# Optimization experiments

Hardware: AMD Instinct MI355X
Metric: run time of the kernel (lower is better)

Reference implementation:

```python
import jax, jax.numpy as jnp
import numpy as np

H, KV, D, HID, FF = 32, 8, 128, 4096, 14336
EPS = 1e-5
ROPE_THETA = 1e9


def setup_inputs() -> dict:
    key = jax.random.key(0)
    ks = jax.random.split(key, 10)
    B, S = 1, 2048
    s = 0.02
    return {
        "hidden_states": jax.random.normal(ks[0], (B, S, HID), dtype=jnp.float32),
        "wq": jax.random.normal(ks[1], (HID, H * D), dtype=jnp.float32) * s,
        "wk": jax.random.normal(ks[2], (HID, KV * D), dtype=jnp.float32) * s,
        "wv": jax.random.normal(ks[3], (HID, KV * D), dtype=jnp.float32) * s,
        "wo": jax.random.normal(ks[4], (H * D, HID), dtype=jnp.float32) * s,
        "w_gate": jax.random.normal(ks[5], (HID, FF), dtype=jnp.float32) * s,
        "w_up": jax.random.normal(ks[6], (HID, FF), dtype=jnp.float32) * s,
        "w_down": jax.random.normal(ks[7], (FF, HID), dtype=jnp.float32) * s,
        "ln1_w": jnp.ones((HID,), dtype=jnp.float32),
        "ln2_w": jnp.ones((HID,), dtype=jnp.float32),
        "position_ids": jnp.arange(B * S, dtype=jnp.int32).reshape(B, S),
    }


def _rmsnorm(x, w):
    var = jnp.mean(jnp.square(x), axis=-1, keepdims=True)
    return x * jax.lax.rsqrt(var + EPS) * w


def _rope_cos_sin(position_ids):
    inv_freq = 1.0 / (ROPE_THETA ** (jnp.arange(0, D, 2, dtype=jnp.float32) / D))  # [D/2]
    ang = position_ids.astype(jnp.float32)[..., None] * inv_freq  # [B,S,D/2]
    ang = jnp.concatenate([ang, ang], axis=-1)  # [B,S,D]
    return jnp.cos(ang), jnp.sin(ang)


def _rotate_half(x):
    x1, x2 = x[..., : D // 2], x[..., D // 2:]
    return jnp.concatenate([-x2, x1], axis=-1)


def _apply_rope(x, cos, sin):
    # x: [B,S,h,D]; cos/sin: [B,S,D]
    c, s = cos[:, :, None, :], sin[:, :, None, :]
    return x * c + _rotate_half(x) * s


def reference(hidden_states, wq, wk, wv, wo, w_gate, w_up, w_down, ln1_w, ln2_w, position_ids):
    B, S, _ = hidden_states.shape
    G = H // KV  # query groups per kv head

    # --- attention block ---
    residual = hidden_states
    x = _rmsnorm(hidden_states, ln1_w)
    q = (x @ wq).reshape(B, S, H, D)
    k = (x @ wk).reshape(B, S, KV, D)
    v = (x @ wv).reshape(B, S, KV, D)

    cos, sin = _rope_cos_sin(position_ids)
    q = _apply_rope(q, cos, sin)
    k = _apply_rope(k, cos, sin)

    # GQA: group query heads over kv heads, [B,S,KV,G,D]
    qg = q.reshape(B, S, KV, G, D)
    scores = jnp.einsum("bqhgd,bkhd->bhgqk", qg, k) / jnp.sqrt(jnp.float32(D))
    causal = position_ids[:, :, None] >= position_ids[:, None, :]  # [B,S,S]
    scores = jnp.where(causal[:, None, None, :, :], scores, jnp.float32(-1e9))
    probs = jax.nn.softmax(scores, axis=-1)
    attn = jnp.einsum("bhgqk,bkhd->bqhgd", probs, v).reshape(B, S, H * D)
    hidden_states = residual + attn @ wo

    # --- MLP block (SwiGLU) ---
    residual = hidden_states
    x = _rmsnorm(hidden_states, ln2_w)
    mlp = (jax.nn.silu(x @ w_gate) * (x @ w_up)) @ w_down
    return residual + mlp
```

## Files before the change

### kernel.cpp

```cpp
#include <hip/hip_runtime.h>

typedef short bf16x8 __attribute__((ext_vector_type(8)));
typedef float f32x4 __attribute__((ext_vector_type(4)));

#define DEV __device__ __forceinline__

constexpr int SEQ = 2048;
constexpr int HID = 4096;
constexpr int NH  = 32;
constexpr int NKV = 8;
constexpr int DH  = 128;
constexpr int FF  = 14336;
constexpr int QKVN = NH * DH + 2 * NKV * DH;

DEV unsigned short f2bf(float f) {
  union { float f; unsigned u; } x; x.f = f;
  unsigned r = x.u + 0x7fffu + ((x.u >> 16) & 1u);
  return (unsigned short)(r >> 16);
}
DEV float bf2f(unsigned short u) {
  union { unsigned u; float f; } x; x.u = ((unsigned)u) << 16; return x.f;
}
DEV void gload16(const void* g, void* l) {
  __builtin_amdgcn_global_load_lds(
      (const __attribute__((address_space(1))) unsigned*)g,
      (__attribute__((address_space(3))) unsigned*)l, 16, 0, 0);
}

DEV void wtrans_tail(char* smbase, int tid, int tile0, int stride,
                     const float* __restrict__ TW,
                     unsigned short* __restrict__ TWT, int TK, int TN) {
  const int team = tid >> 8, lt = tid & 255;
  unsigned short(*tt)[72] = (unsigned short(*)[72])(smbase + team * 9216);
  const int tilesK = TK >> 6;
  const int tot = tilesK * (TN >> 6);
  const int tk = lt >> 4;
  const int tn4 = (lt & 15) * 4;
  for (int tile = tile0 * 2 + team; tile < tot; tile += stride * 2) {
    const int k0 = (tile % tilesK) << 6;
    const int n0t = (tile / tilesK) << 6;
#pragma unroll
    for (int p = 0; p < 4; ++p) {
      int k = tk + p * 16;
      float4 v = *(const float4*)(TW + (size_t)(k0 + k) * TN + n0t + tn4);
      tt[tn4 + 0][k] = f2bf(v.x);
      tt[tn4 + 1][k] = f2bf(v.y);
      tt[tn4 + 2][k] = f2bf(v.z);
      tt[tn4 + 3][k] = f2bf(v.w);
    }
    __syncthreads();
#pragma unroll
    for (int p = 0; p < 4; ++p) {
      int n = tk + p * 16;
      ushort4 o = *(const ushort4*)&tt[n][tn4];
      *(ushort4*)(TWT + (size_t)(n0t + n) * TK + k0 + tn4) = o;
    }
    __syncthreads();
  }
}

__global__ __launch_bounds__(256) void rmsnorm_kernel(
    const float* __restrict__ x, const float* __restrict__ w,
    unsigned short* __restrict__ out) {
  const int row = blockIdx.x;
  const int tid = threadIdx.x;
  const float* xr = x + (size_t)row * HID;
  float4 v[4];
  float ss = 0.f;
#pragma unroll
  for (int i = 0; i < 4; ++i) {
    v[i] = *(const float4*)(xr + i * 1024 + tid * 4);
    ss += v[i].x * v[i].x + v[i].y * v[i].y + v[i].z * v[i].z + v[i].w * v[i].w;
  }
#pragma unroll
  for (int m = 1; m < 64; m <<= 1) ss += __shfl_xor(ss, m);
  __shared__ float red[4];
  if ((tid & 63) == 0) red[tid >> 6] = ss;
  __syncthreads();
  float tot = red[0] + red[1] + red[2] + red[3];
  float rms = rsqrtf(tot / (float)HID + 1e-5f);
  unsigned short* orow = out + (size_t)row * HID;
#pragma unroll
  for (int i = 0; i < 4; ++i) {
    int base = i * 1024 + tid * 4;
    ushort4 o;
    o.x = f2bf(v[i].x * rms * w[base + 0]);
    o.y = f2bf(v[i].y * rms * w[base + 1]);
    o.z = f2bf(v[i].z * rms * w[base + 2]);
    o.w = f2bf(v[i].w * rms * w[base + 3]);
    *(ushort4*)(orow + base) = o;
  }
}

__global__ __launch_bounds__(256) void wtrans_kernel(
    const float* __restrict__ W, unsigned short* __restrict__ WT, int K,
    int N) {
  __shared__ unsigned short t[64][72];
  const int k0 = blockIdx.x * 64, n0 = blockIdx.y * 64;
  const int tid = threadIdx.x;
  const int tk = tid >> 4;
  const int tn4 = (tid & 15) * 4;
#pragma unroll
  for (int p = 0; p < 4; ++p) {
    int k = tk + p * 16;
    float4 v = *(const float4*)(W + (size_t)(k0 + k) * N + n0 + tn4);
    t[tn4 + 0][k] = f2bf(v.x);
    t[tn4 + 1][k] = f2bf(v.y);
    t[tn4 + 2][k] = f2bf(v.z);
    t[tn4 + 3][k] = f2bf(v.w);
  }
  __syncthreads();
#pragma unroll
  for (int p = 0; p < 4; ++p) {
    int n = tk + p * 16;
    ushort4 o = *(const ushort4*)&t[n][tn4];
    *(ushort4*)(WT + (size_t)(n0 + n) * K + k0 + tn4) = o;
  }
}

__global__ __launch_bounds__(256) void rope_kernel(unsigned short* __restrict__ x,
                                                   int nheads, int ld) {
  const int gid = blockIdx.x * 256 + threadIdx.x;
  const int i = gid & 63;
  const int t = gid >> 6;
  const int s = t / nheads;
  const int hh = t - s * nheads;
  float ang = (float)s * exp2f((float)i * (-29.897352853986263f / 64.f));
  float sn, cs;
  sincosf(ang, &sn, &cs);
  size_t base = (size_t)s * ld + hh * DH + i;
  float x1 = bf2f(x[base]);
  float x2 = bf2f(x[base + 64]);
  x[base]      = f2bf(x1 * cs - x2 * sn);
  x[base + 64] = f2bf(x2 * cs + x1 * sn);
}

__global__ __launch_bounds__(256) void combine_kernel(
    const float* __restrict__ p0, const float* __restrict__ p1,
    const float* __restrict__ res, float* __restrict__ out) {
  const size_t i = ((size_t)blockIdx.x * 256 + threadIdx.x) * 4;
  float4 a = *(const float4*)(p0 + i);
  float4 b = *(const float4*)(p1 + i);
  float4 c = *(const float4*)(res + i);
  float4 o;
  o.x = a.x + b.x + c.x;
  o.y = a.y + b.y + c.y;
  o.z = a.z + b.z + c.z;
  o.w = a.w + b.w + c.w;
  *(float4*)(out + i) = o;
}

__global__ __launch_bounds__(256) void combine_rms_kernel(
    const float* __restrict__ p0, const float* __restrict__ p1,
    const float* __restrict__ res, const float* __restrict__ w,
    float* __restrict__ h2, unsigned short* __restrict__ xn2) {
  const int row = blockIdx.x;
  const int tid = threadIdx.x;
  const size_t base = (size_t)row * HID;
  float4 h[4];
  float ss = 0.f;
#pragma unroll
  for (int i = 0; i < 4; ++i) {
    size_t idx = base + i * 1024 + tid * 4;
    float4 a = *(const float4*)(p0 + idx);
    float4 b = *(const float4*)(p1 + idx);
    float4 c = *(const float4*)(res + idx);
    h[i].x = a.x + b.x + c.x;
    h[i].y = a.y + b.y + c.y;
    h[i].z = a.z + b.z + c.z;
    h[i].w = a.w + b.w + c.w;
    *(float4*)(h2 + idx) = h[i];
    ss += h[i].x * h[i].x + h[i].y * h[i].y + h[i].z * h[i].z + h[i].w * h[i].w;
  }
#pragma unroll
  for (int m = 1; m < 64; m <<= 1) ss += __shfl_xor(ss, m);
  __shared__ float red[4];
  if ((tid & 63) == 0) red[tid >> 6] = ss;
  __syncthreads();
  float tot = red[0] + red[1] + red[2] + red[3];
  float rms = rsqrtf(tot / (float)HID + 1e-5f);
#pragma unroll
  for (int i = 0; i < 4; ++i) {
    int off = i * 1024 + tid * 4;
    ushort4 o;
    o.x = f2bf(h[i].x * rms * w[off + 0]);
    o.y = f2bf(h[i].y * rms * w[off + 1]);
    o.z = f2bf(h[i].z * rms * w[off + 2]);
    o.w = f2bf(h[i].w * rms * w[off + 3]);
    *(ushort4*)(xn2 + base + off) = o;
  }
}

template <int EPI>
__global__ __launch_bounds__(512, 2) void gemm8p_kernel(
    const unsigned short* __restrict__ A, const unsigned short* __restrict__ BT,
    void* __restrict__ Cv0, void* __restrict__ Cv1, int gridM, int N, int Kld,
    int nsplit, const float* __restrict__ TW, unsigned short* __restrict__ TWT,
    int TK, int TN, int n_t) {
  constexpr int MF = 4;
  constexpr int ABYTES = 256 * 128;
  constexpr int BUFBYTES = ABYTES + 32768;
  __shared__ __align__(128) char sm[2 * BUFBYTES];

  const int tid = threadIdx.x;
  const int nwg = gridDim.x - n_t;

  if ((int)blockIdx.x >= nwg) {
    wtrans_tail(sm, tid, (int)blockIdx.x - nwg, n_t, TW, TWT, TK, TN);
    return;
  }

  const int lane = tid & 63;
  const int wv   = tid >> 6;
  const int b = blockIdx.x;
  const int logical = (b & 7) * (nwg >> 3) + (b >> 3);
  const int ntiles = nwg / nsplit;
  const int s = logical / ntiles;
  const int r = logical - s * ntiles;
  const int m0 = (r % gridM) * 256;
  const int n0 = (r / gridM) * 256;
  const int Klen = Kld / nsplit;
  const int koff = s * Klen;
  const int wm = (wv >> 2) * 128;
  const int wn = (wv & 3) * 64;
  const int nt = Klen >> 6;

  const int srow = tid >> 3;
  const int scolb = (tid & 7) * 16;
  const int sldsbase = wv * 1024;

  auto stage = [&](int h, int t) {
    const int buf = t & 1;
    const int kt = koff + t * 64;
    char* ldsOp;
    const unsigned short* g;
    int grow0, rowBase;
    if (h < 2) {
      ldsOp = sm + buf * BUFBYTES + ABYTES; g = BT; grow0 = n0; rowBase = h * 128;
    } else {
      ldsOp = sm + buf * BUFBYTES;          g = A;  grow0 = m0; rowBase = (h - 2) * 128;
    }
#pragma unroll
    for (int rr = 0; rr < 2; ++rr) {
      int row = rowBase + rr * 64 + srow;
      const char* gp = (const char*)g + ((size_t)(grow0 + row) * Kld + kt) * 2 +
                       (scolb ^ ((row & 7) << 4));
      gload16(gp, ldsOp + rowBase * 128 + rr * 8192 + sldsbase);
    }
  };

  const int kb0 = (lane >> 4) * 16;
  const int lrow = lane & 15;
  auto ldA = [&](const char* sA, int mh, int mf, int ks) {
    int row = wm + mh * 64 + mf * 16 + lrow;
    return *(const bf16x8*)(sA + ((row * 128 + kb0 + ks * 64) ^ ((row & 7) << 4)));
  };
  auto ldB = [&](const char* sB, int j, int ks) {
    int col = wn + j * 16 + lrow;
    return *(const bf16x8*)(sB + ((col * 128 + kb0 + ks * 64) ^ ((col & 7) << 4)));
  };

  f32x4 acc[2 * MF][4] = {};

  stage(2, 0); stage(3, 0); stage(0, 0); stage(1, 0);
  if (nt > 1) {
    stage(0, 1); stage(1, 1);
    asm volatile("s_waitcnt vmcnt(4)" ::: "memory");
  } else {
    asm volatile("s_waitcnt vmcnt(0)" ::: "memory");
  }
  __builtin_amdgcn_s_barrier();

  for (int t = 0; t < nt; ++t) {
    const char* sA = sm + (t & 1) * BUFBYTES;
    const char* sB = sA + ABYTES;
    bf16x8 a[MF], bb[4][2];

#pragma unroll
    for (int j = 0; j < 4; ++j) bb[j][0] = ldB(sB, j, 0);
#pragma unroll
    for (int mf = 0; mf < MF; ++mf) a[mf] = ldA(sA, 0, mf, 0);
    if (t + 1 < nt) stage(2, t + 1);
    __builtin_amdgcn_sched_barrier(0);
    __builtin_amdgcn_s_barrier();
    __builtin_amdgcn_s_setprio(1);
#pragma unroll
    for (int mf = 0; mf < MF; ++mf)
#pragma unroll
      for (int j = 0; j < 4; ++j)
        acc[mf][j] = __builtin_amdgcn_mfma_f32_16x16x32_bf16(
            a[mf], bb[j][0], acc[mf][j], 0, 0, 0);
    __builtin_amdgcn_s_setprio(0);
    __builtin_amdgcn_sched_barrier(0);
    __builtin_amdgcn_s_barrier();

#pragma unroll
    for (int j = 0; j < 4; ++j) bb[j][1] = ldB(sB, j, 1);
#pragma unroll
    for (int mf = 0; mf < MF; ++mf) a[mf] = ldA(sA, 0, mf, 1);
    if (t + 1 < nt) stage(3, t + 1);
    __builtin_amdgcn_sched_barrier(0);
    __builtin_amdgcn_s_barrier();
    __builtin_amdgcn_s_setprio(1);
#pragma unroll
    for (int mf = 0; mf < MF; ++mf)
#pragma unroll
      for (int j = 0; j < 4; ++j)
        acc[mf][j] = __builtin_amdgcn_mfma_f32_16x16x32_bf16(
            a[mf], bb[j][1], acc[mf][j], 0, 0, 0);
    __builtin_amdgcn_s_setprio(0);
    __builtin_amdgcn_sched_barrier(0);
    __builtin_amdgcn_s_barrier();

#pragma unroll
    for (int mf = 0; mf < MF; ++mf) a[mf] = ldA(sA, 1, mf, 0);
    if (t + 2 < nt) stage(0, t + 2);
    __builtin_amdgcn_sched_barrier(0);
    __builtin_amdgcn_s_barrier();
    __builtin_amdgcn_s_setprio(1);
#pragma unroll
    for (int mf = 0; mf < MF; ++mf)
#pragma unroll
      for (int j = 0; j < 4; ++j)
        acc[MF + mf][j] = __builtin_amdgcn_mfma_f32_16x16x32_bf16(
            a[mf], bb[j][0], acc[MF + mf][j], 0, 0, 0);
    __builtin_amdgcn_s_setprio(0);
    __builtin_amdgcn_sched_barrier(0);
    __builtin_amdgcn_s_barrier();

#pragma unroll
    for (int mf = 0; mf < MF; ++mf) a[mf] = ldA(sA, 1, mf, 1);
    if (t + 2 < nt) {
      stage(1, t + 2);
      asm volatile("s_waitcnt vmcnt(4)" ::: "memory");
    } else {
      asm volatile("s_waitcnt vmcnt(0)" ::: "memory");
    }
    __builtin_amdgcn_sched_barrier(0);
    __builtin_amdgcn_s_barrier();
    __builtin_amdgcn_s_setprio(1);
#pragma unroll
    for (int mf = 0; mf < MF; ++mf)
#pragma unroll
      for (int j = 0; j < 4; ++j)
        acc[MF + mf][j] = __builtin_amdgcn_mfma_f32_16x16x32_bf16(
            a[mf], bb[j][1], acc[MF + mf][j], 0, 0, 0);
    __builtin_amdgcn_s_setprio(0);
    __builtin_amdgcn_sched_barrier(0);
    __builtin_amdgcn_s_barrier();
  }

  const int rb = (lane >> 4) * 4;
  float* P = (float*)(s ? Cv1 : Cv0);
#pragma unroll
  for (int i = 0; i < 2 * MF; ++i) {
    const int mh = i / MF, mf = i % MF;
#pragma unroll
    for (int j = 0; j < 4; ++j) {
#pragma unroll
      for (int rr = 0; rr < 4; ++rr) {
        size_t row = (size_t)(m0 + wm + mh * 64 + mf * 16 + rb + rr);
        size_t col = (size_t)(n0 + wn + j * 16 + lrow);
        float vv = acc[i][j][rr];
        if (EPI == 0) {
          ((unsigned short*)Cv0)[row * N + col] = f2bf(vv);
        } else if (EPI == 2) {
          P[row * N + col] = vv;
        } else {
          float g = bf2f(((const unsigned short*)Cv1)[row * N + col]);
          float sl = g / (1.f + __expf(-g));
          ((unsigned short*)Cv0)[row * N + col] = f2bf(sl * vv);
        }
      }
    }
  }
}

__global__ __launch_bounds__(512, 1) void attn_kernel(
    const unsigned short* __restrict__ QKV, unsigned short* __restrict__ Ob,
    const float* __restrict__ TW, unsigned short* __restrict__ TWT, int TK,
    int TN, int n_t) {
  __shared__ __align__(128) char sm[114688];
  const int tid  = threadIdx.x;
  const int nattn = gridDim.x - n_t;
  if ((int)blockIdx.x >= nattn) {
    wtrans_tail(sm, tid, (int)blockIdx.x - nattn, n_t, TW, TWT, TK, TN);
    return;
  }
  char* sQ  = sm;
  char* sK0 = sm + 32768;
  char* sK1 = sm + 49152;
  char* sV0 = sm + 65536;
  char* sV1 = sm + 81920;
  char* sP  = sm + 98304;
  const int lane = tid & 63;
  const int wv   = tid >> 6;
  const int logical = blockIdx.x;
  const int xr = 15 - (logical >> 5);
  const int h = logical & 31;
  const int qb0 = xr * 128;
  const int hkv = h >> 2;
  const int rbase = (lane >> 4) * 4;
  const int cbase = lane & 15;
  const unsigned short* Qp = QKV + h * DH;
  const unsigned short* Kp = QKV + NH * DH + hkv * DH;
  const unsigned short* Vp = QKV + NH * DH + NKV * DH + hkv * DH;

#pragma unroll
  for (int i = 0; i < 4; ++i) {
    int offs = i * 8192 + tid * 16;
    int row = offs >> 8, col = offs & 255;
    const char* gp = (const char*)Qp + ((size_t)(qb0 + row) * QKVN) * 2 +
                     (col ^ ((row & 15) << 4));
    gload16(gp, sQ + i * 8192 + wv * 1024);
  }

  auto stageK = [&](int t) {
    char* dst = (t & 1) ? sK1 : sK0;
    const int kt0 = t * 64;
#pragma unroll
    for (int i = 0; i < 2; ++i) {
      int offs = i * 8192 + tid * 16;
      int row = offs >> 8, col = offs & 255;
      const char* gp = (const char*)Kp + ((size_t)(kt0 + row) * QKVN) * 2 +
                       (col ^ ((row & 15) << 4));
      gload16(gp, dst + i * 8192 + wv * 1024);
    }
  };

  const int d4  = (tid & 31) * 4;
  const int kv4 = (tid >> 5) * 4;
  const int rot = (tid >> 1) & 3;
  auto loadV = [&](int t, ushort4* vr) {
    const unsigned short* g0 = Vp + (size_t)(t * 64 + kv4) * QKVN + d4;
#pragma unroll
    for (int k = 0; k < 4; ++k) vr[k] = *(const ushort4*)(g0 + (size_t)k * QKVN);
  };
  auto writeV = [&](int t, const ushort4* vr) {
    char* dst = (t & 1) ? sV1 : sV0;
    const unsigned short* a0 = (const unsigned short*)&vr[0];
    const unsigned short* a1 = (const unsigned short*)&vr[1];
    const unsigned short* a2 = (const unsigned short*)&vr[2];
    const unsigned short* a3 = (const unsigned short*)&vr[3];
#pragma unroll
    for (int j = 0; j < 4; ++j) {
      int jj = (j + rot) & 3;
      int dd = d4 + jj;
      uint2 pk;
      pk.x = (unsigned)a0[jj] | ((unsigned)a1[jj] << 16);
      pk.y = (unsigned)a2[jj] | ((unsigned)a3[jj] << 16);
      *(uint2*)(dst + ((dd * 128 + kv4 * 2) ^ ((dd & 7) << 4))) = pk;
    }
  };

  ushort4 vr[4];
  stageK(0);
  loadV(0, vr);
  asm volatile("s_waitcnt vmcnt(0)" ::: "memory");
  writeV(0, vr);
  __syncthreads();

  const int qrow = wv * 16 + (lane & 15);
  bf16x8 aq[4];
#pragma unroll
  for (int kk = 0; kk < 4; ++kk) {
    int kb = (lane >> 4) * 16 + kk * 64;
    aq[kk] = *(const bf16x8*)(sQ + ((qrow * 256 + kb) ^ ((qrow & 15) << 4)));
  }

  f32x4 oacc[8] = {};
  float m_r[4] = {-1e30f, -1e30f, -1e30f, -1e30f};
  float l_r[4] = {0.f, 0.f, 0.f, 0.f};
  const int ntiles = 2 * (xr + 1);

  for (int t = 0; t < ntiles; ++t) {
    const int kt0 = t * 64;
    const char* cK = (t & 1) ? sK1 : sK0;
    const char* cV = (t & 1) ? sV1 : sV0;
    if (t + 1 < ntiles) {
      stageK(t + 1);
      loadV(t + 1, vr);
    }

    f32x4 sacc[4] = {};
#pragma unroll
    for (int kk = 0; kk < 4; ++kk) {
      int kb = (lane >> 4) * 16 + kk * 64;
#pragma unroll
      for (int ni = 0; ni < 4; ++ni) {
        int krow = ni * 16 + (lane & 15);
        bf16x8 bk =
            *(const bf16x8*)(cK + ((krow * 256 + kb) ^ ((krow & 15) << 4)));
        sacc[ni] = __builtin_amdgcn_mfma_f32_16x16x32_bf16(aq[kk], bk,
                                                           sacc[ni], 0, 0, 0);
      }
    }

    const float scale = 0.08838834764831845f;
#pragma unroll
    for (int r = 0; r < 4; ++r) {
      int qg = qb0 + wv * 16 + rbase + r;
      float mx = -1e30f;
#pragma unroll
      for (int ni = 0; ni < 4; ++ni) {
        int cg = kt0 + ni * 16 + cbase;
        float sv = sacc[ni][r] * scale;
        sv = (cg <= qg) ? sv : -1e30f;
        sacc[ni][r] = sv;
        mx = fmaxf(mx, sv);
      }
      mx = fmaxf(mx, __shfl_xor(mx, 1));
      mx = fmaxf(mx, __shfl_xor(mx, 2));
      mx = fmaxf(mx, __shfl_xor(mx, 4));
      mx = fmaxf(mx, __shfl_xor(mx, 8));
      float mnew = fmaxf(m_r[r], mx);
      float sf = __expf(m_r[r] - mnew);
      m_r[r] = mnew;
      float rsum = 0.f;
#pragma unroll
      for (int ni = 0; ni < 4; ++ni) {
        float pv = __expf(sacc[ni][r] - mnew);
        sacc[ni][r] = pv;
        rsum += pv;
      }
      rsum += __shfl_xor(rsum, 1);
      rsum += __shfl_xor(rsum, 2);
      rsum += __shfl_xor(rsum, 4);
      rsum += __shfl_xor(rsum, 8);
      l_r[r] = l_r[r] * sf + rsum;
#pragma unroll
      for (int nt2 = 0; nt2 < 8; ++nt2) oacc[nt2][r] *= sf;
    }

    char* pw = sP + wv * 2048;
#pragma unroll
    for (int ni = 0; ni < 4; ++ni)
#pragma unroll
      for (int r = 0; r < 4; ++r) {
        int row = rbase + r;
        int cb2 = (ni * 16 + cbase) * 2;
        *(unsigned short*)(pw + ((row * 128 + cb2) ^ ((row & 7) << 4))) =
            f2bf(sacc[ni][r]);
      }
    asm volatile("s_waitcnt lgkmcnt(0)" ::: "memory");

#pragma unroll
    for (int kk = 0; kk < 2; ++kk) {
      int kb = (lane >> 4) * 16 + kk * 64;
      int prow = lane & 15;
      bf16x8 ap =
          *(const bf16x8*)(pw + ((prow * 128 + kb) ^ ((prow & 7) << 4)));
#pragma unroll
      for (int nt2 = 0; nt2 < 8; ++nt2) {
        int vrow = nt2 * 16 + (lane & 15);
        bf16x8 bv =
            *(const bf16x8*)(cV + ((vrow * 128 + kb) ^ ((vrow & 7) << 4)));
        oacc[nt2] =
            __builtin_amdgcn_mfma_f32_16x16x32_bf16(ap, bv, oacc[nt2], 0, 0, 0);
      }
    }

    if (t + 1 < ntiles) {
      asm volatile("s_waitcnt vmcnt(0)" ::: "memory");
      writeV(t + 1, vr);
    }
    __syncthreads();
  }

#pragma unroll
  for (int nt2 = 0; nt2 < 8; ++nt2)
#pragma unroll
    for (int r = 0; r < 4; ++r) {
      size_t row = (size_t)(qb0 + wv * 16 + rbase + r);
      int col = nt2 * 16 + cbase;
      Ob[row * (NH * DH) + h * DH + col] = f2bf(oacc[nt2][r] / l_r[r]);
    }
}

extern "C" void kernel_launch(void* const* d_in, const int* in_sizes, int n_in,
                              void* d_out, int out_size, void* d_ws,
                              size_t ws_size, hipStream_t stream) {
  const float* hs  = (const float*)d_in[0];
  const float* wq  = (const float*)d_in[1];
  const float* wk  = (const float*)d_in[2];
  const float* wvp = (const float*)d_in[3];
  const float* wo  = (const float*)d_in[4];
  const float* wg  = (const float*)d_in[5];
  const float* wu  = (const float*)d_in[6];
  const float* wd  = (const float*)d_in[7];
  const float* ln1 = (const float*)d_in[8];
  const float* ln2 = (const float*)d_in[9];

  char* p = (char*)d_ws;
  size_t need = 0;
  auto alloc = [&](size_t bytes) {
    char* r = p + need;
    need += (bytes + 255) & ~(size_t)255;
    return r;
  };
  unsigned short* T1   = (unsigned short*)alloc((size_t)FF * HID * 2);
  unsigned short* xn   = (unsigned short*)alloc((size_t)SEQ * HID * 2);
  unsigned short* qkv  = (unsigned short*)alloc((size_t)SEQ * QKVN * 2);
  unsigned short* ab   = (unsigned short*)alloc((size_t)SEQ * NH * DH * 2);
  float*          h2   = (float*)alloc((size_t)SEQ * HID * 4);
  unsigned short* xn2  = (unsigned short*)alloc((size_t)SEQ * HID * 2);
  unsigned short* gbuf = (unsigned short*)alloc((size_t)SEQ * FF * 2);
  unsigned short* ubuf = (unsigned short*)alloc((size_t)SEQ * FF * 2);
  size_t need_base = need;
  unsigned short* T2   = (unsigned short*)alloc((size_t)FF * HID * 2);
  const bool fat = (ws_size >= need);
  if (ws_size < need_base) return;

  float* pO0 = (float*)gbuf;
  float* pO1 = (float*)xn;
  float* pD0 = fat ? (float*)T2 : (float*)ubuf;
  float* pD1 = fat ? (float*)(T2 + (size_t)SEQ * HID * 2) : (float*)xn;
  (void)ubuf;

  rmsnorm_kernel<<<SEQ, 256, 0, stream>>>(hs, ln1, xn);
  wtrans_kernel<<<dim3(HID / 64, HID / 64), 256, 0, stream>>>(wq, T1, HID, HID);
  wtrans_kernel<<<dim3(HID / 64, (NKV * DH) / 64), 256, 0, stream>>>(
      wk, T1 + (size_t)(NH * DH) * HID, HID, NKV * DH);
  wtrans_kernel<<<dim3(HID / 64, (NKV * DH) / 64), 256, 0, stream>>>(
      wvp, T1 + (size_t)(NH * DH + NKV * DH) * HID, HID, NKV * DH);
  if (fat) {
    gemm8p_kernel<0><<<192 + 64, 512, 0, stream>>>(
        xn, T1, qkv, nullptr, SEQ / 256, QKVN, HID, 1, wo, T2, HID, HID, 64);
  } else {
    gemm8p_kernel<0><<<192, 512, 0, stream>>>(
        xn, T1, qkv, nullptr, SEQ / 256, QKVN, HID, 1, nullptr, nullptr, 64, 64, 0);
  }
  rope_kernel<<<(SEQ * (NH + NKV) * 64) / 256, 256, 0, stream>>>(qkv, NH + NKV,
                                                                 QKVN);
  if (fat) {
    attn_kernel<<<512 + 512, 512, 0, stream>>>(qkv, ab, wg, T1, HID, FF, 512);
  } else {
    attn_kernel<<<512, 512, 0, stream>>>(qkv, ab, nullptr, nullptr, 64, 64, 0);
  }
  unsigned short* Wo = fat ? T2 : T1;
  if (!fat)
    wtrans_kernel<<<dim3(HID / 64, HID / 64), 256, 0, stream>>>(wo, T1, HID, HID);
  gemm8p_kernel<2><<<256, 512, 0, stream>>>(
      ab, Wo, pO0, pO1, SEQ / 256, HID, HID, 2, nullptr, nullptr, 64, 64, 0);
  combine_rms_kernel<<<SEQ, 256, 0, stream>>>(pO0, pO1, hs, ln2, h2, xn2);
  if (fat) {
    gemm8p_kernel<0><<<448 + 1024, 512, 0, stream>>>(
        xn2, T1, gbuf, nullptr, SEQ / 256, FF, HID, 1, wu, T2, HID, FF, 1024);
  } else {
    wtrans_kernel<<<dim3(HID / 64, FF / 64), 256, 0, stream>>>(wg, T1, HID, FF);
    gemm8p_kernel<0><<<448, 512, 0, stream>>>(
        xn2, T1, gbuf, nullptr, SEQ / 256, FF, HID, 1, nullptr, nullptr, 64, 64, 0);
  }
  if (fat) {
    gemm8p_kernel<3><<<448 + 1024, 512, 0, stream>>>(
        xn2, T2, gbuf, gbuf, SEQ / 256, FF, HID, 1, wd, T1, FF, HID, 1024);
  } else {
    wtrans_kernel<<<dim3(HID / 64, FF / 64), 256, 0, stream>>>(wu, T1, HID, FF);
    gemm8p_kernel<3><<<448, 512, 0, stream>>>(
        xn2, T1, gbuf, gbuf, SEQ / 256, FF, HID, 1, nullptr, nullptr, 64, 64, 0);
  }
  if (!fat)
    wtrans_kernel<<<dim3(FF / 64, HID / 64), 256, 0, stream>>>(wd, T1, FF, HID);
  gemm8p_kernel<2><<<256, 512, 0, stream>>>(
      gbuf, T1, pD0, pD1, SEQ / 256, HID, FF, 2, nullptr, nullptr, 64, 64, 0);
  combine_kernel<<<(SEQ * HID) / 1024, 256, 0, stream>>>(pD0, pD1, h2,
                                                         (float*)d_out);
}
```

Baseline: 1.225 ms.

## Triple-buffer K tiles in attention and skip online-softmax rescale when max stable

The attention kernel now keeps three K tile buffers in shared memory and prefetches K two tiles ahead, so a K load has more time to land behind compute. The wait before writing V is relaxed to vmcnt(2), so the newer K loads can stay in flight. It also adds lazy online-softmax rescaling: the running max only moves when the tile max exceeds it by more than 5, which lets the output-accumulator rescale be skipped when no lane needs it. This raises shared memory use to 128 KB per block and risks overflow or precision loss if exp values reach up to e^5 above the stored max in the accumulation.

Result: no change. 1.233 ms (+0.7%).

```diff
diff --git a/kernel.cpp b/kernel.cpp
--- a/kernel.cpp
+++ b/kernel.cpp
@@ -380,7 +380,7 @@
     const unsigned short* __restrict__ QKV, unsigned short* __restrict__ Ob,
     const float* __restrict__ TW, unsigned short* __restrict__ TWT, int TK,
     int TN, int n_t) {
-  __shared__ __align__(128) char sm[114688];
+  __shared__ __align__(128) char sm[131072];
   const int tid  = threadIdx.x;
   const int nattn = gridDim.x - n_t;
   if ((int)blockIdx.x >= nattn) {
@@ -388,11 +388,9 @@
     return;
   }
   char* sQ  = sm;
-  char* sK0 = sm + 32768;
-  char* sK1 = sm + 49152;
-  char* sV0 = sm + 65536;
-  char* sV1 = sm + 81920;
-  char* sP  = sm + 98304;
+  char* sKb = sm + 32768;
+  char* sVb = sm + 81920;
+  char* sP  = sm + 114688;
   const int lane = tid & 63;
   const int wv   = tid >> 6;
   const int logical = blockIdx.x;
@@ -416,7 +414,7 @@
   }
 
   auto stageK = [&](int t) {
-    char* dst = (t & 1) ? sK1 : sK0;
+    char* dst = sKb + (t % 3) * 16384;
     const int kt0 = t * 64;
 #pragma unroll
     for (int i = 0; i < 2; ++i) {
@@ -437,7 +435,7 @@
     for (int k = 0; k < 4; ++k) vr[k] = *(const ushort4*)(g0 + (size_t)k * QKVN);
   };
   auto writeV = [&](int t, const ushort4* vr) {
-    char* dst = (t & 1) ? sV1 : sV0;
+    char* dst = sVb + (t & 1) * 16384;
     const unsigned short* a0 = (const unsigned short*)&vr[0];
     const unsigned short* a1 = (const unsigned short*)&vr[1];
     const unsigned short* a2 = (const unsigned short*)&vr[2];
@@ -453,11 +451,13 @@
     }
   };
 
+  const int ntiles = 2 * (xr + 1);
   ushort4 vr[4];
   stageK(0);
   loadV(0, vr);
   asm volatile("s_waitcnt vmcnt(0)" ::: "memory");
   writeV(0, vr);
+  if (ntiles > 1) stageK(1);
   __syncthreads();
 
   const int qrow = wv * 16 + (lane & 15);
@@ -471,16 +471,13 @@
   f32x4 oacc[8] = {};
   float m_r[4] = {-1e30f, -1e30f, -1e30f, -1e30f};
   float l_r[4] = {0.f, 0.f, 0.f, 0.f};
-  const int ntiles = 2 * (xr + 1);
 
   for (int t = 0; t < ntiles; ++t) {
     const int kt0 = t * 64;
-    const char* cK = (t & 1) ? sK1 : sK0;
-    const char* cV = (t & 1) ? sV1 : sV0;
-    if (t + 1 < ntiles) {
-      stageK(t + 1);
-      loadV(t + 1, vr);
-    }
+    const char* cK = sKb + (t % 3) * 16384;
+    const char* cV = sVb + (t & 1) * 16384;
+    if (t + 1 < ntiles) loadV(t + 1, vr);
+    if (t + 2 < ntiles) stageK(t + 2);
 
     f32x4 sacc[4] = {};
 #pragma unroll
@@ -497,6 +494,8 @@
     }
 
     const float scale = 0.08838834764831845f;
+    float sfv[4];
+    bool anyresc = false;
 #pragma unroll
     for (int r = 0; r < 4; ++r) {
       int qg = qb0 + wv * 16 + rbase + r;
@@ -513,8 +512,11 @@
       mx = fmaxf(mx, __shfl_xor(mx, 2));
       mx = fmaxf(mx, __shfl_xor(mx, 4));
       mx = fmaxf(mx, __shfl_xor(mx, 8));
-      float mnew = fmaxf(m_r[r], mx);
-      float sf = __expf(m_r[r] - mnew);
+      bool grew = mx > m_r[r] + 5.0f;
+      float mnew = grew ? mx : m_r[r];
+      float sf = grew ? __expf(m_r[r] - mnew) : 1.0f;
+      sfv[r] = sf;
+      anyresc |= grew;
       m_r[r] = mnew;
       float rsum = 0.f;
 #pragma unroll
@@ -528,8 +530,12 @@
       rsum += __shfl_xor(rsum, 4);
       rsum += __shfl_xor(rsum, 8);
       l_r[r] = l_r[r] * sf + rsum;
-#pragma unroll
-      for (int nt2 = 0; nt2 < 8; ++nt2) oacc[nt2][r] *= sf;
+    }
+    if (__any(anyresc)) {
+#pragma unroll
+      for (int nt2 = 0; nt2 < 8; ++nt2)
+#pragma unroll
+        for (int r = 0; r < 4; ++r) oacc[nt2][r] *= sfv[r];
     }
 
     char* pw = sP + wv * 2048;
@@ -561,7 +567,10 @@
     }
 
     if (t + 1 < ntiles) {
-      asm volatile("s_waitcnt vmcnt(0)" ::: "memory");
+      if (t + 2 < ntiles)
+        asm volatile("s_waitcnt vmcnt(2)" ::: "memory");
+      else
+        asm volatile("s_waitcnt vmcnt(0)" ::: "memory");
       writeV(t + 1, vr);
     }
     __syncthreads();
```
